# Kernel tuning notes

Measured on AMD Instinct MI355X. Metric: run time of the kernel, lower is better.

Reference implementation:

```python
import jax, jax.numpy as jnp
import numpy as np

N_NODES = 100000
N_EDGES = 300000
D = 256
N_LAYERS = 4
BN_EPS = 1e-5


def setup_inputs() -> dict:
    key = jax.random.key(0)
    ks = jax.random.split(key, 6)
    x = jax.random.normal(ks[0], (N_NODES, D), dtype=jnp.float32)
    rows = jax.random.randint(ks[1], (N_EDGES,), 0, N_NODES)
    cols = jax.random.randint(ks[2], (N_EDGES,), 0, N_NODES)
    vals = jax.random.uniform(ks[3], (N_EDGES,), dtype=jnp.float32)
    stdv = 1.0 / np.sqrt(D).astype(np.float32)
    weights = jax.random.uniform(ks[4], (N_LAYERS, D, D), jnp.float32, -stdv, stdv)
    self_weights = jax.random.uniform(ks[5], (N_LAYERS, D, D), jnp.float32, -stdv, stdv)
    gammas = jnp.ones((N_LAYERS, D), jnp.float32)
    betas = jnp.zeros((N_LAYERS, D), jnp.float32)
    return {"x": x, "vals": vals, "weights": weights, "self_weights": self_weights,
            "gammas": gammas, "betas": betas, "rows": rows, "cols": cols}


def reference(x, vals, weights, self_weights, gammas, betas, rows, cols):
    n = x.shape[0]

    def gcn_layer(h, W, SW, gamma, beta):
        # support = h @ W  -> dense [N, D]
        support = h @ W
        # spmm(adj, support): out[i] = sum_{e: rows[e]==i} vals[e] * support[cols[e]]
        agg = jax.ops.segment_sum(vals[:, None] * support[cols], rows, num_segments=n)
        out = agg + h @ SW  # self-loop term (withloop=True)
        # BatchNorm1d over nodes (training-mode batch stats, biased variance)
        mean = out.mean(axis=0)
        var = out.var(axis=0)
        out = gamma * (out - mean) * jax.lax.rsqrt(var + BN_EPS) + beta
        return jax.nn.relu(out)

    h = x
    for i in range(N_LAYERS):
        h = gcn_layer(h, weights[i], self_weights[i], gammas[i], betas[i])
    # aggrmethod='concat', dense=False -> cat(final, input)
    return jnp.concatenate([h, x], axis=1)
```

## Files before the change

### kernel.cpp

```cpp
#include <hip/hip_runtime.h>
#include <hip/hip_bf16.h>
#include <stdint.h>

#define M_NODES 100000
#define NE      300000
#define D       256
#define D2      512
#define NLAYERS 4

#define SPMM_CHUNK 16

typedef float  f32x4  __attribute__((ext_vector_type(4)));
typedef __bf16 bf16x8 __attribute__((ext_vector_type(8)));

static __device__ __forceinline__ float bf2f(uint32_t u) {
  union { uint32_t i; float f; } v; v.i = u << 16; return v.f;
}
static __device__ __forceinline__ uint32_t f2bf(float f) {
  union { float f; uint32_t i; } v; v.f = f;
  return (v.i + 0x7fffu + ((v.i >> 16) & 1u)) >> 16;
}
static __device__ __forceinline__ void gload_lds16(const void* g, void* l) {
  __builtin_amdgcn_global_load_lds((const __attribute__((address_space(1))) uint32_t*)g,
                                   (__attribute__((address_space(3))) uint32_t*)l, 16, 0, 0);
}

__global__ void hist_kernel(const int* __restrict__ rows, int* __restrict__ counts) {
  int e = blockIdx.x * 256 + threadIdx.x;
  if (e < NE) atomicAdd(&counts[rows[e]], 1);
}

__global__ void scan1_kernel(const int* __restrict__ counts, int* __restrict__ rp,
                             int* __restrict__ bsum) {
  __shared__ int sd[256];
  int tid = threadIdx.x;
  int base = blockIdx.x * 1024 + tid * 4;
  int v0 = (base + 0 < M_NODES) ? counts[base + 0] : 0;
  int v1 = (base + 1 < M_NODES) ? counts[base + 1] : 0;
  int v2 = (base + 2 < M_NODES) ? counts[base + 2] : 0;
  int v3 = (base + 3 < M_NODES) ? counts[base + 3] : 0;
  int tsum = v0 + v1 + v2 + v3;
  sd[tid] = tsum; __syncthreads();
  for (int off = 1; off < 256; off <<= 1) {
    int x = sd[tid];
    if (tid >= off) x += sd[tid - off];
    __syncthreads(); sd[tid] = x; __syncthreads();
  }
  int excl = sd[tid] - tsum;
  if (base + 0 < M_NODES) rp[base + 0] = excl; excl += v0;
  if (base + 1 < M_NODES) rp[base + 1] = excl; excl += v1;
  if (base + 2 < M_NODES) rp[base + 2] = excl; excl += v2;
  if (base + 3 < M_NODES) rp[base + 3] = excl;
  if (tid == 255) bsum[blockIdx.x] = sd[255];
}

__global__ void scan2_kernel(const int* __restrict__ bsum, int* __restrict__ boff) {
  __shared__ int sd[128];
  int tid = threadIdx.x;
  int v = (tid < 98) ? bsum[tid] : 0;
  sd[tid] = v; __syncthreads();
  for (int off = 1; off < 128; off <<= 1) {
    int x = sd[tid];
    if (tid >= off) x += sd[tid - off];
    __syncthreads(); sd[tid] = x; __syncthreads();
  }
  if (tid < 98) boff[tid] = sd[tid] - v;
}

__global__ void scan3_kernel(int* __restrict__ rp, const int* __restrict__ boff,
                             int* __restrict__ cursor) {
  int i = blockIdx.x * 256 + threadIdx.x;
  if (i > M_NODES) return;
  int v = (i < M_NODES) ? rp[i] + boff[i >> 10] : NE;
  rp[i] = v;
  if (i < M_NODES) cursor[i] = v;
}

__global__ void scatter_kernel(const int* __restrict__ rows, const int* __restrict__ cols,
                               const float* __restrict__ vals, int* __restrict__ cursor,
                               uint2* __restrict__ emeta) {
  int e = blockIdx.x * 256 + threadIdx.x;
  if (e >= NE) return;
  int r = rows[e];
  int p = atomicAdd(&cursor[r], 1);
  uint2 m; m.x = (uint32_t)cols[e]; m.y = __float_as_uint(vals[e]);
  emeta[p] = m;
}

__global__ void conv_w_kernel(const float* __restrict__ W, const float* __restrict__ SW,
                              ushort* __restrict__ Bt) {
  int idx = blockIdx.x * 256 + threadIdx.x;
  if (idx >= NLAYERS * D2 * D) return;
  int k = idx & (D - 1);
  int n = (idx >> 8) & (D2 - 1);
  int layer = idx >> 17;
  float v = (n < D) ? W[(size_t)layer * D * D + k * D + n]
                    : SW[(size_t)layer * D * D + k * D + (n - D)];
  Bt[idx] = (ushort)f2bf(v);
}

#define BM 128
#define BN 128
#define BK 64
#define MTILES 782
#define MTILES_PAD 784
#define GEMM_GRID (MTILES_PAD * 4)

template<int MODE>
__global__ __launch_bounds__(256, 4)
void gemm_kernel(const float* __restrict__ x, const ushort* __restrict__ P,
                 const float* __restrict__ stats, const float* __restrict__ gamma,
                 const float* __restrict__ beta, const ushort* __restrict__ Bt,
                 ushort* __restrict__ outAB, float* __restrict__ out) {
  const int bid = blockIdx.x;
  const int mr = bid & 7;
  const int nb = (bid >> 3) & 3;
  const int mt = (bid >> 5) * 8 + mr;
  if (mt >= MTILES) return;
  const int m0 = mt * BM;
  const int n0 = nb * BN;

  __shared__ __align__(16) ushort smem[BM * BK + BN * BK];
  ushort* As = smem;
  ushort* Bs = smem + BM * BK;
  const int tid = threadIdx.x;
  const int wv = tid >> 6, l = tid & 63;
  const int wr = wv >> 1, wc = wv & 1;
  const int lrow = l & 15, lhi = l >> 4;

  f32x4 acc[4][4] = {};

  const int arow = tid >> 3;
  const int acb  = (tid & 7) << 4;
  const int acol = acb >> 1;

#pragma unroll
  for (int s = 0; s < 4; ++s) {
    const int k0 = s * BK;
    float sc[8], sh[8];
    if (MODE == 1) {
      float sm[8], sq[8], gg[8], bb[8];
      *(float4*)(sm)     = *(const float4*)(stats + k0 + acol);
      *(float4*)(sm + 4) = *(const float4*)(stats + k0 + acol + 4);
      *(float4*)(sq)     = *(const float4*)(stats + D + k0 + acol);
      *(float4*)(sq + 4) = *(const float4*)(stats + D + k0 + acol + 4);
      *(float4*)(gg)     = *(const float4*)(gamma + k0 + acol);
      *(float4*)(gg + 4) = *(const float4*)(gamma + k0 + acol + 4);
      *(float4*)(bb)     = *(const float4*)(beta + k0 + acol);
      *(float4*)(bb + 4) = *(const float4*)(beta + k0 + acol + 4);
#pragma unroll
      for (int k = 0; k < 8; ++k) {
        float mean = sm[k] * (1.0f / M_NODES);
        float var  = sq[k] * (1.0f / M_NODES) - mean * mean;
        float rstd = rsqrtf(var + 1e-5f);
        sc[k] = gg[k] * rstd;
        sh[k] = bb[k] - mean * sc[k];
      }
    }
#pragma unroll
    for (int p = 0; p < 4; ++p) {
      int row = p * 32 + arow;
      int grow = m0 + row;
      const bool inb = grow < M_NODES;
      if (!inb) grow = M_NODES - 1;
      float f[8];
      if (MODE == 0) {
        float4 v0 = *(const float4*)(x + (size_t)grow * D + k0 + acol);
        float4 v1 = *(const float4*)(x + (size_t)grow * D + k0 + acol + 4);
        f[0] = v0.x; f[1] = v0.y; f[2] = v0.z; f[3] = v0.w;
        f[4] = v1.x; f[5] = v1.y; f[6] = v1.z; f[7] = v1.w;
        if (nb == 0 && inb) {
          *(float4*)(out + (size_t)grow * D2 + D + k0 + acol) = v0;
          *(float4*)(out + (size_t)grow * D2 + D + k0 + acol + 4) = v1;
        }
      } else {
        uint4 u = *(const uint4*)(P + (size_t)grow * D + k0 + acol);
        f[0] = fmaxf(bf2f(u.x & 0xffff) * sc[0] + sh[0], 0.f);
        f[1] = fmaxf(bf2f(u.x >> 16)    * sc[1] + sh[1], 0.f);
        f[2] = fmaxf(bf2f(u.y & 0xffff) * sc[2] + sh[2], 0.f);
        f[3] = fmaxf(bf2f(u.y >> 16)    * sc[3] + sh[3], 0.f);
        f[4] = fmaxf(bf2f(u.z & 0xffff) * sc[4] + sh[4], 0.f);
        f[5] = fmaxf(bf2f(u.z >> 16)    * sc[5] + sh[5], 0.f);
        f[6] = fmaxf(bf2f(u.w & 0xffff) * sc[6] + sh[6], 0.f);
        f[7] = fmaxf(bf2f(u.w >> 16)    * sc[7] + sh[7], 0.f);
      }
      uint4 o;
      o.x = f2bf(f[0]) | (f2bf(f[1]) << 16);
      o.y = f2bf(f[2]) | (f2bf(f[3]) << 16);
      o.z = f2bf(f[4]) | (f2bf(f[5]) << 16);
      o.w = f2bf(f[6]) | (f2bf(f[7]) << 16);
      *(uint4*)((char*)As + row * 128 + (acb ^ ((row & 7) << 4))) = o;
    }
#pragma unroll
    for (int p = 0; p < 4; ++p) {
      int row = p * 32 + arow;
      int gn = n0 + row;
      int gcb = acb ^ ((row & 7) << 4);
      gload_lds16(Bt + (size_t)gn * D + k0 + (gcb >> 1), Bs + row * BK + (acb >> 1));
    }
    __syncthreads();
#pragma unroll
    for (int kk = 0; kk < 2; ++kk) {
      bf16x8 af[4], bfr[4];
#pragma unroll
      for (int mi = 0; mi < 4; ++mi) {
        int row = wr * 64 + mi * 16 + lrow;
        int off = row * 128 + ((kk * 64 + lhi * 16) ^ ((row & 7) << 4));
        af[mi] = *(const bf16x8*)((const char*)As + off);
      }
#pragma unroll
      for (int nj = 0; nj < 4; ++nj) {
        int row = wc * 64 + nj * 16 + lrow;
        int off = row * 128 + ((kk * 64 + lhi * 16) ^ ((row & 7) << 4));
        bfr[nj] = *(const bf16x8*)((const char*)Bs + off);
      }
#pragma unroll
      for (int mi = 0; mi < 4; ++mi)
#pragma unroll
        for (int nj = 0; nj < 4; ++nj)
          acc[mi][nj] = __builtin_amdgcn_mfma_f32_16x16x32_bf16(af[mi], bfr[nj], acc[mi][nj], 0, 0, 0);
    }
    __syncthreads();
  }

#pragma unroll
  for (int mi = 0; mi < 4; ++mi)
#pragma unroll
    for (int nj = 0; nj < 4; ++nj)
#pragma unroll
      for (int r = 0; r < 4; ++r) {
        int rl = wr * 64 + mi * 16 + lhi * 4 + r;
        int cl = wc * 64 + nj * 16 + lrow;
        smem[rl * 128 + (cl ^ ((rl & 7) << 3))] = (ushort)f2bf(acc[mi][nj][r]);
      }
  __syncthreads();
  const int rg = tid >> 4, lc16 = tid & 15;
#pragma unroll
  for (int i = 0; i < 8; ++i) {
    int rl = i * 16 + rg;
    int grow = m0 + rl;
    if (grow < M_NODES) {
      uint4 v = *(const uint4*)(smem + rl * 128 + ((lc16 * 8) ^ ((rl & 7) << 3)));
      *(uint4*)(outAB + (size_t)grow * D2 + n0 + lc16 * 8) = v;
    }
  }
}

__global__ __launch_bounds__(256, 8)
void spmm_kernel(const ushort* __restrict__ AB, ushort* __restrict__ P,
                 const int* __restrict__ rp, const uint2* __restrict__ emeta,
                 float* __restrict__ stats) {
  __shared__ float sstats[2 * D];
  for (int i = threadIdx.x; i < 2 * D; i += 256) sstats[i] = 0.f;
  __syncthreads();

  const int wv = threadIdx.x >> 6, l = threadIdx.x & 63;
  const int wave = blockIdx.x * 4 + wv;
  const int row0 = wave * SPMM_CHUNK;

  float s0 = 0, s1 = 0, s2 = 0, s3 = 0, q0 = 0, q1 = 0, q2 = 0, q3 = 0;

  if (row0 < M_NODES) {
    const int nrows = (M_NODES - row0 < SPMM_CHUNK) ? (M_NODES - row0) : SPMM_CHUNK;
    int myrp = (l <= nrows) ? rp[row0 + l] : 0;
    const int ebase = __shfl(myrp, 0);
    const int ecnt  = __shfl(myrp, nrows) - ebase;
    uint2 m0 = {0u, 0u}, m1 = {0u, 0u};
    if (l < ecnt)      m0 = emeta[ebase + l];
    if (64 + l < ecnt) m1 = emeta[ebase + 64 + l];

    for (int t = 0; t < nrows; ++t) {
      const int i = row0 + t;
      const int e0 = __shfl(myrp, t);
      const int e1 = __shfl(myrp, t + 1);
      const int deg = e1 - e0;

      const ushort4 st = *(const ushort4*)(AB + (size_t)i * D2 + D + 4 * l);
      float a0 = bf2f(st.x), a1 = bf2f(st.y), a2 = bf2f(st.z), a3 = bf2f(st.w);

      for (int b = 0; b < deg; b += 4) {
        float vv[4]; ushort4 sp[4];
#pragma unroll
        for (int j = 0; j < 4; ++j) {
          int ej = b + j;
          int ecl = (ej < deg) ? ej : (deg - 1);
          int slot = e0 - ebase + ecl;
          int sl = slot & 63;
          int cA = __shfl((int)m0.x, sl);
          int cB = __shfl((int)m1.x, sl);
          float vA = __shfl(__uint_as_float(m0.y), sl);
          float vB = __shfl(__uint_as_float(m1.y), sl);
          int   c = (slot < 64) ? cA : cB;
          float v = (slot < 64) ? vA : vB;
          if (slot >= 128 && ej < deg) {
            uint2 m = emeta[e0 + ecl]; c = (int)m.x; v = __uint_as_float(m.y);
          }
          vv[j] = (ej < deg) ? v : 0.f;
          sp[j] = *(const ushort4*)(AB + (size_t)c * D2 + 4 * l);
        }
#pragma unroll
        for (int j = 0; j < 4; ++j) {
          a0 += vv[j] * bf2f(sp[j].x); a1 += vv[j] * bf2f(sp[j].y);
          a2 += vv[j] * bf2f(sp[j].z); a3 += vv[j] * bf2f(sp[j].w);
        }
      }

      ushort4 o;
      o.x = (ushort)f2bf(a0); o.y = (ushort)f2bf(a1);
      o.z = (ushort)f2bf(a2); o.w = (ushort)f2bf(a3);
      *(ushort4*)(P + (size_t)i * D + 4 * l) = o;
      s0 += a0; q0 += a0 * a0; s1 += a1; q1 += a1 * a1;
      s2 += a2; q2 += a2 * a2; s3 += a3; q3 += a3 * a3;
    }
  }

  const int c0 = 4 * l;
  atomicAdd(&sstats[c0 + 0], s0); atomicAdd(&sstats[c0 + 1], s1);
  atomicAdd(&sstats[c0 + 2], s2); atomicAdd(&sstats[c0 + 3], s3);
  atomicAdd(&sstats[D + c0 + 0], q0); atomicAdd(&sstats[D + c0 + 1], q1);
  atomicAdd(&sstats[D + c0 + 2], q2); atomicAdd(&sstats[D + c0 + 3], q3);
  __syncthreads();
  atomicAdd(&stats[threadIdx.x], sstats[threadIdx.x]);
  atomicAdd(&stats[D + threadIdx.x], sstats[D + threadIdx.x]);
}

__global__ void norm_last_kernel(const ushort* __restrict__ P, const float* __restrict__ stats,
                                 const float* __restrict__ gamma, const float* __restrict__ beta,
                                 float* __restrict__ out) {
  const int cs = threadIdx.x & 31;
  const int rr = threadIdx.x >> 5;
  const int c0 = cs * 8;

  float sc[8], sh[8];
#pragma unroll
  for (int k = 0; k < 8; ++k) {
    float mean = stats[c0 + k] * (1.0f / M_NODES);
    float var  = stats[D + c0 + k] * (1.0f / M_NODES) - mean * mean;
    float rstd = rsqrtf(var + 1e-5f);
    float g = gamma[c0 + k];
    sc[k] = g * rstd;
    sh[k] = beta[c0 + k] - mean * sc[k];
  }

  const int r0 = blockIdx.x * 64;
#pragma unroll
  for (int rb = 0; rb < 8; ++rb) {
    int r = r0 + rb * 8 + rr;
    if (r >= M_NODES) break;
    const uint4 u = *(const uint4*)(P + (size_t)r * D + c0);
    float f[8];
    f[0] = bf2f(u.x & 0xffff); f[1] = bf2f(u.x >> 16);
    f[2] = bf2f(u.y & 0xffff); f[3] = bf2f(u.y >> 16);
    f[4] = bf2f(u.z & 0xffff); f[5] = bf2f(u.z >> 16);
    f[6] = bf2f(u.w & 0xffff); f[7] = bf2f(u.w >> 16);
#pragma unroll
    for (int k = 0; k < 8; ++k) f[k] = fmaxf(f[k] * sc[k] + sh[k], 0.f);
    float4 r0v = { f[0], f[1], f[2], f[3] };
    float4 r1v = { f[4], f[5], f[6], f[7] };
    *(float4*)(out + (size_t)r * D2 + c0) = r0v;
    *(float4*)(out + (size_t)r * D2 + c0 + 4) = r1v;
  }
}

extern "C" void kernel_launch(void* const* d_in, const int* in_sizes, int n_in,
                              void* d_out, int out_size, void* d_ws, size_t ws_size,
                              hipStream_t stream) {
  const float* x      = (const float*)d_in[0];
  const float* vals   = (const float*)d_in[1];
  const float* W      = (const float*)d_in[2];
  const float* SW     = (const float*)d_in[3];
  const float* gammas = (const float*)d_in[4];
  const float* betas  = (const float*)d_in[5];
  const int*   rows   = (const int*)d_in[6];
  const int*   cols   = (const int*)d_in[7];
  float* out = (float*)d_out;

  char* ws = (char*)d_ws;
  size_t off = 0;
  auto alloc = [&](size_t bytes) {
    void* p = ws + off;
    off = (off + bytes + 255) & ~(size_t)255;
    return p;
  };
  ushort* AB     = (ushort*)alloc((size_t)M_NODES * D2 * 2);
  ushort* P      = (ushort*)alloc((size_t)M_NODES * D * 2);
  ushort* Bt     = (ushort*)alloc((size_t)NLAYERS * D2 * D * 2);
  int*    rp     = (int*)alloc((M_NODES + 1) * 4);
  int*    cursor = (int*)alloc((M_NODES + 1) * 4);
  uint2*  emeta  = (uint2*)alloc((size_t)NE * 8);
  int*    bsum   = (int*)alloc(512);
  int*    boff   = (int*)alloc(512);
  float*  stats  = (float*)alloc(NLAYERS * 2 * D * 4);

  hipMemsetAsync(cursor, 0, (size_t)M_NODES * 4, stream);
  hipMemsetAsync(stats, 0, (size_t)NLAYERS * 2 * D * 4, stream);

  hist_kernel<<<(NE + 255) / 256, 256, 0, stream>>>(rows, cursor);
  scan1_kernel<<<98, 256, 0, stream>>>(cursor, rp, bsum);
  scan2_kernel<<<1, 128, 0, stream>>>(bsum, boff);
  scan3_kernel<<<(M_NODES + 256) / 256, 256, 0, stream>>>(rp, boff, cursor);
  scatter_kernel<<<(NE + 255) / 256, 256, 0, stream>>>(rows, cols, vals, cursor, emeta);

  conv_w_kernel<<<(NLAYERS * D2 * D) / 256, 256, 0, stream>>>(W, SW, Bt);

  const int spmm_blocks = (M_NODES + SPMM_CHUNK * 4 - 1) / (SPMM_CHUNK * 4);
  for (int lyr = 0; lyr < NLAYERS; ++lyr) {
    if (lyr == 0)
      gemm_kernel<0><<<GEMM_GRID, 256, 0, stream>>>(x, nullptr, nullptr, nullptr, nullptr,
                                                    Bt + (size_t)lyr * D2 * D, AB, out);
    else
      gemm_kernel<1><<<GEMM_GRID, 256, 0, stream>>>(nullptr, P, stats + (size_t)(lyr - 1) * 2 * D,
                                                    gammas + (size_t)(lyr - 1) * D,
                                                    betas + (size_t)(lyr - 1) * D,
                                                    Bt + (size_t)lyr * D2 * D, AB, nullptr);
    spmm_kernel<<<spmm_blocks, 256, 0, stream>>>(AB, P, rp, emeta,
                                                 stats + (size_t)lyr * 2 * D);
  }
  norm_last_kernel<<<(M_NODES + 63) / 64, 256, 0, stream>>>(
      P, stats + (size_t)(NLAYERS - 1) * 2 * D, gammas + (size_t)(NLAYERS - 1) * D,
      betas + (size_t)(NLAYERS - 1) * D, out);
}
```

Before: 794.6 us.

## Unfuse BN+ReLU from GEMM prologue into separate norm kernel with async LDS loads

Moves the batch-norm/ReLU normalization and fp32-to-bf16 conversion out of the GEMM A-tile load into standalone kernels (prep_x for layer 0, norm_kernel per layer). The GEMM then loads a precomputed bf16 h buffer straight into LDS with global_load_lds, as it already does for B. Before, every one of the four N-block tiles redid the normalization and loaded A through registers. This costs an extra read and write of the 100000x256 bf16 activation per layer plus extra kernel launches.

New measurement: 714.9 us. -10.0%, faster.

```diff
diff --git a/kernel.cpp b/kernel.cpp
--- a/kernel.cpp
+++ b/kernel.cpp
@@ -87,6 +87,18 @@
   emeta[p] = m;
 }
 
+__global__ void prep_x_kernel(const float* __restrict__ x, ushort* __restrict__ h,
+                              float* __restrict__ out) {
+  size_t idx = (size_t)blockIdx.x * 256 + threadIdx.x;
+  size_t i = idx >> 6; int c = (int)(idx & 63) * 4;
+  float4 v = *(const float4*)(x + i * D + c);
+  *(float4*)(out + i * D2 + D + c) = v;
+  ushort4 o;
+  o.x = (ushort)f2bf(v.x); o.y = (ushort)f2bf(v.y);
+  o.z = (ushort)f2bf(v.z); o.w = (ushort)f2bf(v.w);
+  *(ushort4*)(h + i * D + c) = o;
+}
+
 __global__ void conv_w_kernel(const float* __restrict__ W, const float* __restrict__ SW,
                               ushort* __restrict__ Bt) {
   int idx = blockIdx.x * 256 + threadIdx.x;
@@ -106,12 +118,9 @@
 #define MTILES_PAD 784
 #define GEMM_GRID (MTILES_PAD * 4)
 
-template<int MODE>
 __global__ __launch_bounds__(256, 4)
-void gemm_kernel(const float* __restrict__ x, const ushort* __restrict__ P,
-                 const float* __restrict__ stats, const float* __restrict__ gamma,
-                 const float* __restrict__ beta, const ushort* __restrict__ Bt,
-                 ushort* __restrict__ outAB, float* __restrict__ out) {
+void gemm_kernel(const ushort* __restrict__ h, const ushort* __restrict__ Bt,
+                 ushort* __restrict__ outAB) {
   const int bid = blockIdx.x;
   const int mr = bid & 7;
   const int nb = (bid >> 3) & 3;
@@ -132,64 +141,16 @@
 
   const int arow = tid >> 3;
   const int acb  = (tid & 7) << 4;
-  const int acol = acb >> 1;
 
 #pragma unroll
   for (int s = 0; s < 4; ++s) {
     const int k0 = s * BK;
-    float sc[8], sh[8];
-    if (MODE == 1) {
-      float sm[8], sq[8], gg[8], bb[8];
-      *(float4*)(sm)     = *(const float4*)(stats + k0 + acol);
-      *(float4*)(sm + 4) = *(const float4*)(stats + k0 + acol + 4);
-      *(float4*)(sq)     = *(const float4*)(stats + D + k0 + acol);
-      *(float4*)(sq + 4) = *(const float4*)(stats + D + k0 + acol + 4);
-      *(float4*)(gg)     = *(const float4*)(gamma + k0 + acol);
-      *(float4*)(gg + 4) = *(const float4*)(gamma + k0 + acol + 4);
-      *(float4*)(bb)     = *(const float4*)(beta + k0 + acol);
-      *(float4*)(bb + 4) = *(const float4*)(beta + k0 + acol + 4);
-#pragma unroll
-      for (int k = 0; k < 8; ++k) {
-        float mean = sm[k] * (1.0f / M_NODES);
-        float var  = sq[k] * (1.0f / M_NODES) - mean * mean;
-        float rstd = rsqrtf(var + 1e-5f);
-        sc[k] = gg[k] * rstd;
-        sh[k] = bb[k] - mean * sc[k];
-      }
-    }
 #pragma unroll
     for (int p = 0; p < 4; ++p) {
       int row = p * 32 + arow;
-      int grow = m0 + row;
-      const bool inb = grow < M_NODES;
-      if (!inb) grow = M_NODES - 1;
-      float f[8];
-      if (MODE == 0) {
-        float4 v0 = *(const float4*)(x + (size_t)grow * D + k0 + acol);
-        float4 v1 = *(const float4*)(x + (size_t)grow * D + k0 + acol + 4);
-        f[0] = v0.x; f[1] = v0.y; f[2] = v0.z; f[3] = v0.w;
-        f[4] = v1.x; f[5] = v1.y; f[6] = v1.z; f[7] = v1.w;
-        if (nb == 0 && inb) {
-          *(float4*)(out + (size_t)grow * D2 + D + k0 + acol) = v0;
-          *(float4*)(out + (size_t)grow * D2 + D + k0 + acol + 4) = v1;
-        }
-      } else {
-        uint4 u = *(const uint4*)(P + (size_t)grow * D + k0 + acol);
-        f[0] = fmaxf(bf2f(u.x & 0xffff) * sc[0] + sh[0], 0.f);
-        f[1] = fmaxf(bf2f(u.x >> 16)    * sc[1] + sh[1], 0.f);
-        f[2] = fmaxf(bf2f(u.y & 0xffff) * sc[2] + sh[2], 0.f);
-        f[3] = fmaxf(bf2f(u.y >> 16)    * sc[3] + sh[3], 0.f);
-        f[4] = fmaxf(bf2f(u.z & 0xffff) * sc[4] + sh[4], 0.f);
-        f[5] = fmaxf(bf2f(u.z >> 16)    * sc[5] + sh[5], 0.f);
-        f[6] = fmaxf(bf2f(u.w & 0xffff) * sc[6] + sh[6], 0.f);
-        f[7] = fmaxf(bf2f(u.w >> 16)    * sc[7] + sh[7], 0.f);
-      }
-      uint4 o;
-      o.x = f2bf(f[0]) | (f2bf(f[1]) << 16);
-      o.y = f2bf(f[2]) | (f2bf(f[3]) << 16);
-      o.z = f2bf(f[4]) | (f2bf(f[5]) << 16);
-      o.w = f2bf(f[6]) | (f2bf(f[7]) << 16);
-      *(uint4*)((char*)As + row * 128 + (acb ^ ((row & 7) << 4))) = o;
+      int grow = m0 + row; if (grow >= M_NODES) grow = M_NODES - 1;
+      int gcb = acb ^ ((row & 7) << 4);
+      gload_lds16(h + (size_t)grow * D + k0 + (gcb >> 1), As + row * BK + (acb >> 1));
     }
 #pragma unroll
     for (int p = 0; p < 4; ++p) {
@@ -324,9 +285,10 @@
   atomicAdd(&stats[D + threadIdx.x], sstats[D + threadIdx.x]);
 }
 
-__global__ void norm_last_kernel(const ushort* __restrict__ P, const float* __restrict__ stats,
-                                 const float* __restrict__ gamma, const float* __restrict__ beta,
-                                 float* __restrict__ out) {
+template<bool LAST>
+__global__ void norm_kernel(const ushort* __restrict__ P, const float* __restrict__ stats,
+                            const float* __restrict__ gamma, const float* __restrict__ beta,
+                            ushort* __restrict__ hout, float* __restrict__ out) {
   const int cs = threadIdx.x & 31;
   const int rr = threadIdx.x >> 5;
   const int c0 = cs * 8;
@@ -355,10 +317,19 @@
     f[6] = bf2f(u.w & 0xffff); f[7] = bf2f(u.w >> 16);
 #pragma unroll
     for (int k = 0; k < 8; ++k) f[k] = fmaxf(f[k] * sc[k] + sh[k], 0.f);
-    float4 r0v = { f[0], f[1], f[2], f[3] };
-    float4 r1v = { f[4], f[5], f[6], f[7] };
-    *(float4*)(out + (size_t)r * D2 + c0) = r0v;
-    *(float4*)(out + (size_t)r * D2 + c0 + 4) = r1v;
+    if (LAST) {
+      float4 r0v = { f[0], f[1], f[2], f[3] };
+      float4 r1v = { f[4], f[5], f[6], f[7] };
+      *(float4*)(out + (size_t)r * D2 + c0) = r0v;
+      *(float4*)(out + (size_t)r * D2 + c0 + 4) = r1v;
+    } else {
+      uint4 o;
+      o.x = f2bf(f[0]) | (f2bf(f[1]) << 16);
+      o.y = f2bf(f[2]) | (f2bf(f[3]) << 16);
+      o.z = f2bf(f[4]) | (f2bf(f[5]) << 16);
+      o.w = f2bf(f[6]) | (f2bf(f[7]) << 16);
+      *(uint4*)(hout + (size_t)r * D + c0) = o;
+    }
   }
 }
 
@@ -384,6 +355,7 @@
   };
   ushort* AB     = (ushort*)alloc((size_t)M_NODES * D2 * 2);
   ushort* P      = (ushort*)alloc((size_t)M_NODES * D * 2);
+  ushort* h      = (ushort*)alloc((size_t)M_NODES * D * 2);
   ushort* Bt     = (ushort*)alloc((size_t)NLAYERS * D2 * D * 2);
   int*    rp     = (int*)alloc((M_NODES + 1) * 4);
   int*    cursor = (int*)alloc((M_NODES + 1) * 4);
@@ -401,22 +373,20 @@
   scan3_kernel<<<(M_NODES + 256) / 256, 256, 0, stream>>>(rp, boff, cursor);
   scatter_kernel<<<(NE + 255) / 256, 256, 0, stream>>>(rows, cols, vals, cursor, emeta);
 
+  prep_x_kernel<<<(M_NODES * D / 4) / 256, 256, 0, stream>>>(x, h, out);
   conv_w_kernel<<<(NLAYERS * D2 * D) / 256, 256, 0, stream>>>(W, SW, Bt);
 
   const int spmm_blocks = (M_NODES + SPMM_CHUNK * 4 - 1) / (SPMM_CHUNK * 4);
+  const int norm_blocks = (M_NODES + 63) / 64;
   for (int lyr = 0; lyr < NLAYERS; ++lyr) {
-    if (lyr == 0)
-      gemm_kernel<0><<<GEMM_GRID, 256, 0, stream>>>(x, nullptr, nullptr, nullptr, nullptr,
-                                                    Bt + (size_t)lyr * D2 * D, AB, out);
-    else
-      gemm_kernel<1><<<GEMM_GRID, 256, 0, stream>>>(nullptr, P, stats + (size_t)(lyr - 1) * 2 * D,
-                                                    gammas + (size_t)(lyr - 1) * D,
-                                                    betas + (size_t)(lyr - 1) * D,
-                                                    Bt + (size_t)lyr * D2 * D, AB, nullptr);
+    gemm_kernel<<<GEMM_GRID, 256, 0, stream>>>(h, Bt + (size_t)lyr * D2 * D, AB);
     spmm_kernel<<<spmm_blocks, 256, 0, stream>>>(AB, P, rp, emeta,
                                                  stats + (size_t)lyr * 2 * D);
-  }
-  norm_last_kernel<<<(M_NODES + 63) / 64, 256, 0, stream>>>(
-      P, stats + (size_t)(NLAYERS - 1) * 2 * D, gammas + (size_t)(NLAYERS - 1) * D,
-      betas + (size_t)(NLAYERS - 1) * D, out);
-}
+    if (lyr < NLAYERS - 1)
+      norm_kernel<false><<<norm_blocks, 256, 0, stream>>>(
+          P, stats + (size_t)lyr * 2 * D, gammas + lyr * D, betas + lyr * D, h, nullptr);
+    else
+      norm_kernel<true><<<norm_blocks, 256, 0, stream>>>(
+          P, stats + (size_t)lyr * 2 * D, gammas + lyr * D, betas + lyr * D, nullptr, out);
+  }
+}
```
